# Kernel tuning notes

Measured on AMD Instinct MI355X. Metric: run time of the kernel, lower is better.

Reference implementation:

```python
import jax, jax.numpy as jnp
import numpy as np
from jax import lax

# --- block geometry (matches init_kwargs) ---
B = 8
DIM = 192
HEADS = 6
KEY_DIM = DIM // HEADS  # 32, attn_ratio=1 so d == key_dim and dh == DIM
HX, WX = 32, 32         # search region
HZ, WZ = 16, 16         # template region
T = 1                   # template_number
L = HX * WX + T * HZ * WZ  # 1280 tokens
MLP_HIDDEN = int(DIM * 4.0)
BN_EPS = 1e-5


def _build_bias_idx():
    """Replicates Attention.__init__ global_att=True bias-index construction.
    Unique-offset ids may be permuted vs torch dict-insertion order, which is an
    equivalent reparameterization of the (randomly initialized) bias table."""
    g = np.stack(np.meshgrid(np.arange(HX), np.arange(WX), indexing='ij'), -1).reshape(-1, 2)
    pts = [g]
    for i in range(T):
        r = np.arange(HX + HZ * i, WX + WZ * (i + 1))
        g2 = np.stack(np.meshgrid(r, r, indexing='ij'), -1).reshape(-1, 2)
        pts.append(g2)
    p = np.concatenate(pts, 0)                      # (L, 2)
    off = np.abs(p[:, None, :] - p[None, :, :])     # (L, L, 2)
    key = off[:, :, 0].astype(np.int64) * 4096 + off[:, :, 1]
    uniq, inv = np.unique(key, return_inverse=True)
    return inv.reshape(L, L).astype(np.int32), int(len(uniq))


def setup_inputs() -> dict:
    key = jax.random.key(0)
    ks = jax.random.split(key, 16)
    idx_np, n_off = _build_bias_idx()
    s = 0.02
    return {
        'xz': jax.random.normal(ks[0], (B, L, DIM), jnp.float32),
        'bias_idx': jnp.asarray(idx_np),
        'ln1_g': jnp.ones((DIM,), jnp.float32),
        'ln1_b': jnp.zeros((DIM,), jnp.float32),
        'wqkv': jax.random.normal(ks[1], (DIM, 3 * DIM), jnp.float32) * s,
        'bqkv': jnp.zeros((3 * DIM,), jnp.float32),
        'wproj': jax.random.normal(ks[2], (DIM, DIM), jnp.float32) * s,
        'bproj': jnp.zeros((DIM,), jnp.float32),
        'bias_table': jax.random.normal(ks[3], (HEADS, n_off), jnp.float32) * 0.1,
        'conv_w': jax.random.normal(ks[4], (3, 3, 1, DIM), jnp.float32) * 0.1,  # depthwise HWIO
        'bn_scale': jnp.ones((DIM,), jnp.float32) + jax.random.normal(ks[5], (DIM,), jnp.float32) * 0.01,
        'bn_bias': jax.random.normal(ks[6], (DIM,), jnp.float32) * 0.01,
        'ln2_g': jnp.ones((DIM,), jnp.float32),
        'ln2_b': jnp.zeros((DIM,), jnp.float32),
        'w1': jax.random.normal(ks[7], (DIM, MLP_HIDDEN), jnp.float32) * s,
        'b1': jnp.zeros((MLP_HIDDEN,), jnp.float32),
        'w2': jax.random.normal(ks[8], (MLP_HIDDEN, DIM), jnp.float32) * s,
        'b2': jnp.zeros((DIM,), jnp.float32),
    }


def _layernorm(x, g, b, eps=1e-5):
    mu = jnp.mean(x, -1, keepdims=True)
    var = jnp.mean(jnp.square(x - mu), -1, keepdims=True)
    return (x - mu) * lax.rsqrt(var + eps) * g + b


def reference(xz, bias_idx, ln1_g, ln1_b, wqkv, bqkv, wproj, bproj, bias_table,
              conv_w, bn_scale, bn_bias, ln2_g, ln2_b, w1, b1, w2, b2):
    Bn, N, D = xz.shape
    scale = KEY_DIM ** -0.5
    # --- Attention (LeViT-style with gathered relative-position bias) ---
    h = _layernorm(xz, ln1_g, ln1_b)
    qkv = (h @ wqkv + bqkv).reshape(Bn, N, HEADS, 3 * KEY_DIM)
    q, k, v = jnp.split(qkv, 3, axis=3)            # each (B, N, H, key_dim)
    bias = bias_table[:, bias_idx]                  # (H, N, N) gather
    attn = jnp.einsum('bnhd,bmhd->bhnm', q, k) * scale + bias
    attn = jax.nn.softmax(attn, axis=-1)
    o = jnp.einsum('bhnm,bmhd->bnhd', attn, v).reshape(Bn, N, D)
    xm = xz + o @ wproj + bproj
    # --- depthwise local conv (Conv2d_BN, BN folded to scale/bias) per segment ---
    segs = []
    start = 0
    for (Hh, Ww) in [(HX, WX)] + [(HZ, WZ)] * T:
        xc = xm[:, start:start + Hh * Ww, :].reshape(Bn, Hh, Ww, D)
        xc = lax.conv_general_dilated(
            xc, conv_w, window_strides=(1, 1), padding='SAME',
            dimension_numbers=('NHWC', 'HWIO', 'NHWC'), feature_group_count=D)
        xc = xc * bn_scale + bn_bias
        segs.append(xc.reshape(Bn, Hh * Ww, D))
        start += Hh * Ww
    xm = jnp.concatenate(segs, axis=1)
    # --- MLP with pre-LN (exact GELU, matching nn.GELU default) ---
    m = _layernorm(xm, ln2_g, ln2_b)
    m = jax.nn.gelu(m @ w1 + b1, approximate=False) @ w2 + b2
    return xm + m
```

## Files before the change

kernel.cpp:

```cpp
#include <hip/hip_runtime.h>
#include <hip/hip_bf16.h>

#define BATCH 8
#define LTOK 1280
#define DIMC 192
#define HEADS 6
#define KD 32
#define HID 768
#define NROWS (BATCH*LTOK)

typedef short s16x8 __attribute__((ext_vector_type(8)));
typedef float f32x4 __attribute__((ext_vector_type(4)));
typedef unsigned short u16;

#define QS (0.17677669529663687f * 1.4426950408889634f)
#define L2E 1.4426950408889634f

__device__ __forceinline__ u16 f2bf(float x) {
    unsigned u = __float_as_uint(x);
    u = (u + 0x7FFFu + ((u >> 16) & 1u)) >> 16;
    return (u16)u;
}
__device__ __forceinline__ float bflo(unsigned u) { return __uint_as_float(u << 16); }
__device__ __forceinline__ float bfhi(unsigned u) { return __uint_as_float(u & 0xffff0000u); }
__device__ __forceinline__ float fexp2(float x) { float r; asm("v_exp_f32 %0, %1" : "=v"(r) : "v"(x)); return r; }
__device__ __forceinline__ float frcp(float x)  { float r; asm("v_rcp_f32 %0, %1" : "=v"(r) : "v"(x)); return r; }

__global__ __launch_bounds__(256) void pre_a(const float* __restrict__ w0,
                                             u16* __restrict__ o0,
                                             const float* __restrict__ xz,
                                             const float* __restrict__ ln1g,
                                             const float* __restrict__ ln1b,
                                             u16* __restrict__ hbuf) {
    __shared__ float s[16][17];
    int f = blockIdx.x;
    if (f >= 432) {
        int row = (f - 432) * 4 + (threadIdx.x >> 6);
        int lane = threadIdx.x & 63;
        const float* xr = xz + (size_t)row * DIMC;
        float v0 = xr[lane], v1 = xr[lane + 64], v2 = xr[lane + 128];
        float sm = v0 + v1 + v2;
        float ss = v0 * v0 + v1 * v1 + v2 * v2;
        #pragma unroll
        for (int off = 32; off; off >>= 1) {
            sm += __shfl_xor(sm, off);
            ss += __shfl_xor(ss, off);
        }
        float mu  = sm * (1.0f / DIMC);
        float var = ss * (1.0f / DIMC) - mu * mu;
        float inv = rsqrtf(var + 1e-5f);
        u16* yr = hbuf + (size_t)row * DIMC;
        yr[lane]       = f2bf((v0 - mu) * inv * ln1g[lane]       + ln1b[lane]);
        yr[lane + 64]  = f2bf((v1 - mu) * inv * ln1g[lane + 64]  + ln1b[lane + 64]);
        yr[lane + 128] = f2bf((v2 - mu) * inv * ln1g[lane + 128] + ln1b[lane + 128]);
        return;
    }
    int tn = f % 36, tk = f / 36;
    int tx = threadIdx.x & 15, ty = threadIdx.x >> 4;
    s[ty][tx] = w0[(size_t)(tk * 16 + ty) * 576 + tn * 16 + tx];
    __syncthreads();
    o0[(size_t)(tn * 16 + ty) * 192 + tk * 16 + tx] = f2bf(s[tx][ty]);
}

__global__ __launch_bounds__(256) void qkv_mega(const u16* __restrict__ A,
                                                const u16* __restrict__ Wt,
                                                const float* __restrict__ bias,
                                                u16* __restrict__ qb,
                                                u16* __restrict__ kp,
                                                u16* __restrict__ vp,
                                                const int* __restrict__ bidx,
                                                const float* __restrict__ btab,
                                                int n_off, u16* __restrict__ bmp,
                                                const float* __restrict__ wp,
                                                const float* __restrict__ wf1,
                                                const float* __restrict__ wf2,
                                                u16* __restrict__ op,
                                                u16* __restrict__ of1,
                                                u16* __restrict__ of2) {
    int bid = blockIdx.x;
    if (bid >= 9960) {
        __shared__ float s[16][17];
        int f2 = bid - 9960;
        const float* in; u16* out; int K, N, tn, tk;
        if (f2 < 144)      { in = wp;  out = op;  K = 192; N = 192; tn = f2 % 12; tk = f2 / 12; }
        else if (f2 < 720) { in = wf1; out = of1; K = 192; N = 768; int q = f2 - 144; tn = q % 48; tk = q / 48; }
        else               { in = wf2; out = of2; K = 768; N = 192; int q = f2 - 720; tn = q % 12; tk = q / 12; }
        int tx = threadIdx.x & 15, ty = threadIdx.x >> 4;
        s[ty][tx] = in[(size_t)(tk * 16 + ty) * N + tn * 16 + tx];
        __syncthreads();
        out[(size_t)(tn * 16 + ty) * K + tk * 16 + tx] = f2bf(s[tx][ty]);
        return;
    }
    if (bid >= 360) {
        int fb = bid - 360;
        int qt = fb / 120;
        int rem = fb - qt * 120;
        int T = rem / 6, h = rem - (rem / 6) * 6;
        int tid = threadIdx.x;
        int half = tid >> 7, L = (tid >> 1) & 63, j4 = (tid & 1) * 4;
        int n = qt * 16 + (L & 15);
        int m = T * 64 + half * 32 + ((L >> 4) << 3) + j4;
        int4 iv = *(const int4*)(bidx + (size_t)n * LTOK + m);
        const float* tab = btab + (size_t)h * n_off;
        ushort4 o;
        o.x = f2bf(tab[iv.x] * L2E);
        o.y = f2bf(tab[iv.y] * L2E);
        o.z = f2bf(tab[iv.z] * L2E);
        o.w = f2bf(tab[iv.w] * L2E);
        *(ushort4*)(bmp + (size_t)(h * 80 + qt) * 20480 + T * 1024 + tid * 4) = o;
        return;
    }
    int bx = bid % 9, by = bid / 9;
    int tid = threadIdx.x;
    int L = tid & 63, w = tid >> 6;
    int r = L & 15, g = L >> 4;
    int m0 = by * 256 + w * 64;
    int n0 = bx * 64;

    f32x4 acc[4][4] = {};
    const u16* Ab = A + (size_t)(m0 + r) * 192 + g * 8;
    const u16* Wb = Wt + (size_t)(n0 + r) * 192 + g * 8;
    #pragma unroll 6
    for (int k0 = 0; k0 < 192; k0 += 32) {
        s16x8 af[4];
        #pragma unroll
        for (int mi = 0; mi < 4; ++mi)
            af[mi] = *(const s16x8*)(Ab + (size_t)mi * 16 * 192 + k0);
        #pragma unroll
        for (int nn = 0; nn < 4; ++nn) {
            s16x8 bf = *(const s16x8*)(Wb + (size_t)nn * 16 * 192 + k0);
            #pragma unroll
            for (int mi = 0; mi < 4; ++mi)
                acc[mi][nn] = __builtin_amdgcn_mfma_f32_16x16x32_bf16(af[mi], bf, acc[mi][nn], 0, 0, 0);
        }
    }
    #pragma unroll
    for (int mi = 0; mi < 4; ++mi)
    #pragma unroll
    for (int nn = 0; nn < 4; ++nn) {
        int cb = n0 + nn * 16;
        int h  = cb / 96, c0 = cb % 96;
        int reg = c0 >> 5;
        #pragma unroll
        for (int i = 0; i < 4; ++i) {
            int row = m0 + mi * 16 + g * 4 + i;
            float v = acc[mi][nn][i] + bias[cb + r];
            if (reg == 0) {
                v *= QS;
                qb[(size_t)row * DIMC + h * 32 + (c0 & 31) + r] = f2bf(v);
            } else {
                int b_ = row / LTOK, t = row - b_ * LTOK;
                int T = t >> 5, it = t & 31;
                int d = (c0 & 31) + r;
                if (reg == 1) {
                    int which = (it >> 2) & 1;
                    int ik = ((it >> 3) << 2) | (it & 3);
                    int Lk = ((d >> 3) << 4) + ik;
                    kp[((size_t)(b_ * HEADS + h) * 40 + T) * 1024 + which * 512 + Lk * 8 + (d & 7)] = f2bf(v);
                } else {
                    int Lv = ((it >> 3) << 4) + (d & 15);
                    vp[((size_t)(b_ * HEADS + h) * 40 + T) * 1024 + (d >> 4) * 512 + Lv * 8 + (it & 7)] = f2bf(v);
                }
            }
        }
    }
}

template<int ACT, int RES, int OBF, int K, int MTILE>
__global__ __launch_bounds__(256) void gemm_mfma(const u16* __restrict__ A,
                                                 const u16* __restrict__ Wt,
                                                 const float* __restrict__ bias,
                                                 const float* __restrict__ R,
                                                 void* __restrict__ Cp,
                                                 int N) {
    constexpr int SUB = MTILE / 64;
    int tid = threadIdx.x;
    int L = tid & 63, w = tid >> 6;
    int r = L & 15, g = L >> 4;
    int m0 = blockIdx.y * MTILE + w * (16 * SUB);
    int n0 = blockIdx.x * 64;

    f32x4 acc[SUB][4] = {};
    const u16* Ab = A + (size_t)(m0 + r) * K + g * 8;
    const u16* Wb = Wt + (size_t)(n0 + r) * K + g * 8;
    #pragma unroll 6
    for (int k0 = 0; k0 < K; k0 += 32) {
        s16x8 af[SUB];
        #pragma unroll
        for (int mi = 0; mi < SUB; ++mi)
            af[mi] = *(const s16x8*)(Ab + (size_t)mi * 16 * K + k0);
        #pragma unroll
        for (int nn = 0; nn < 4; ++nn) {
            s16x8 bf = *(const s16x8*)(Wb + (size_t)nn * 16 * K + k0);
            #pragma unroll
            for (int mi = 0; mi < SUB; ++mi)
                acc[mi][nn] = __builtin_amdgcn_mfma_f32_16x16x32_bf16(af[mi], bf, acc[mi][nn], 0, 0, 0);
        }
    }

    #pragma unroll
    for (int mi = 0; mi < SUB; ++mi)
    #pragma unroll
    for (int nn = 0; nn < 4; ++nn) {
        int cb = n0 + nn * 16;
        #pragma unroll
        for (int i = 0; i < 4; ++i) {
            int row = m0 + mi * 16 + g * 4 + i;
            float v = acc[mi][nn][i] + bias[cb + r];
            if (ACT == 1) {
                float u = v;
                float y = 0.7978845608028654f * (u + 0.044715f * u * u * u);
                float e2 = fexp2(y * 2.885390081777927f);
                v = u - u * frcp(e2 + 1.0f);
            }
            if (RES) v += R[(size_t)row * N + cb + r];
            if (OBF) ((u16*)Cp)[(size_t)row * N + cb + r] = f2bf(v);
            else     ((float*)Cp)[(size_t)row * N + cb + r] = v;
        }
    }
}

__global__ __launch_bounds__(256) void attn_mfma(const u16* __restrict__ qb,
                                                 const u16* __restrict__ kp,
                                                 const u16* __restrict__ vp,
                                                 const u16* __restrict__ bmp,
                                                 u16* __restrict__ ob) {
    __shared__ __align__(16) u16 kvs[2][2][2048];
    int tid = threadIdx.x;
    int L = tid & 63, w = tid >> 6;
    int r = L & 15, g = L >> 4;
    int L8 = L * 8;

    int bid = blockIdx.x;
    int work = (bid & 7) * 120 + (bid >> 3);
    int b  = work & 7;
    int hq = work >> 3;
    int qt = (hq % 20) * 4 + w;
    int h  = hq / 20;

    s16x8 qf = *(const s16x8*)(qb + (size_t)(b * LTOK + qt * 16 + r) * DIMC + h * 32 + g * 8);

    int skv = w >> 1, half = w & 1;
    const u16* gs = (skv ? vp : kp) + (size_t)(b * HEADS + h) * 40 * 1024 + L8;
    u16* dst0 = &kvs[0][skv][half * 1024 + L8];
    u16* dst1 = &kvs[1][skv][half * 1024 + L8];

    const u16* bmr = bmp + (size_t)(h * 80 + qt) * 20480 + L8;

    f32x4 acc0 = {0.f, 0.f, 0.f, 0.f}, acc1 = {0.f, 0.f, 0.f, 0.f};
    float lsum = 0.f;

    {
        int4 pA = *(const int4*)(gs + half * 1024);
        int4 pB = *(const int4*)(gs + half * 1024 + 512);
        *(int4*)dst0 = pA;
        *(int4*)(dst0 + 512) = pB;
    }
    int4 cb0 = *(const int4*)(bmr);
    int4 cb1 = *(const int4*)(bmr + 512);
    __syncthreads();

    f32x4 s0, s1, s2, s3;
    {
        const u16* kb = &kvs[0][0][0];
        f32x4 z0, z1, z2, z3;
        z0[0] = bflo(cb0.x); z0[1] = bfhi(cb0.x); z0[2] = bflo(cb0.y); z0[3] = bfhi(cb0.y);
        z1[0] = bflo(cb0.z); z1[1] = bfhi(cb0.z); z1[2] = bflo(cb0.w); z1[3] = bfhi(cb0.w);
        z2[0] = bflo(cb1.x); z2[1] = bfhi(cb1.x); z2[2] = bflo(cb1.y); z2[3] = bfhi(cb1.y);
        z3[0] = bflo(cb1.z); z3[1] = bfhi(cb1.z); z3[2] = bflo(cb1.w); z3[3] = bfhi(cb1.w);
        s16x8 kf0 = *(const s16x8*)(kb + L8);
        s16x8 kf1 = *(const s16x8*)(kb + 512 + L8);
        s16x8 kf2 = *(const s16x8*)(kb + 1024 + L8);
        s16x8 kf3 = *(const s16x8*)(kb + 1536 + L8);
        s0 = __builtin_amdgcn_mfma_f32_16x16x32_bf16(kf0, qf, z0, 0, 0, 0);
        s1 = __builtin_amdgcn_mfma_f32_16x16x32_bf16(kf1, qf, z1, 0, 0, 0);
        s2 = __builtin_amdgcn_mfma_f32_16x16x32_bf16(kf2, qf, z2, 0, 0, 0);
        s3 = __builtin_amdgcn_mfma_f32_16x16x32_bf16(kf3, qf, z3, 0, 0, 0);
    }

    #pragma unroll 1
    for (int T = 0; T < 20; ++T) {
        int4 nA, nB, nb0, nb1;
        if (T < 19) {
            nA  = *(const int4*)(gs + (size_t)(2 * T + 2 + half) * 1024);
            nB  = *(const int4*)(gs + (size_t)(2 * T + 2 + half) * 1024 + 512);
            nb0 = *(const int4*)(bmr + (size_t)(T + 1) * 1024);
            nb1 = *(const int4*)(bmr + (size_t)(T + 1) * 1024 + 512);
        }
        __builtin_amdgcn_s_setprio(1);
        float p[16];
        #pragma unroll
        for (int j = 0; j < 4; ++j) {
            p[j]      = fexp2(s0[j]);
            p[4 + j]  = fexp2(s1[j]);
            p[8 + j]  = fexp2(s2[j]);
            p[12 + j] = fexp2(s3[j]);
        }
        float t0 = ((p[0] + p[1]) + (p[2] + p[3])) + ((p[4] + p[5]) + (p[6] + p[7]));
        float t1 = ((p[8] + p[9]) + (p[10] + p[11])) + ((p[12] + p[13]) + (p[14] + p[15]));
        lsum += t0 + t1;
        union { unsigned u[4]; s16x8 v; } pa, pb;
        #pragma unroll
        for (int j = 0; j < 4; ++j) {
            asm("v_cvt_pk_bf16_f32 %0, %1, %2" : "=v"(pa.u[j]) : "v"(p[2 * j]), "v"(p[2 * j + 1]));
            asm("v_cvt_pk_bf16_f32 %0, %1, %2" : "=v"(pb.u[j]) : "v"(p[8 + 2 * j]), "v"(p[9 + 2 * j]));
        }
        const u16* vb = &kvs[T & 1][1][0];
        s16x8 v0 = *(const s16x8*)(vb + L8);
        s16x8 v1 = *(const s16x8*)(vb + 512 + L8);
        s16x8 v2 = *(const s16x8*)(vb + 1024 + L8);
        s16x8 v3 = *(const s16x8*)(vb + 1536 + L8);
        acc0 = __builtin_amdgcn_mfma_f32_16x16x32_bf16(pa.v, v0, acc0, 0, 0, 0);
        acc1 = __builtin_amdgcn_mfma_f32_16x16x32_bf16(pa.v, v1, acc1, 0, 0, 0);
        acc0 = __builtin_amdgcn_mfma_f32_16x16x32_bf16(pb.v, v2, acc0, 0, 0, 0);
        acc1 = __builtin_amdgcn_mfma_f32_16x16x32_bf16(pb.v, v3, acc1, 0, 0, 0);
        __builtin_amdgcn_s_setprio(0);

        if (T < 19) {
            u16* d = (T & 1) ? dst0 : dst1;
            *(int4*)d = nA;
            *(int4*)(d + 512) = nB;
        }
        __syncthreads();
        if (T < 19) {
            const u16* kb = &kvs[(T + 1) & 1][0][0];
            f32x4 z0, z1, z2, z3;
            z0[0] = bflo(nb0.x); z0[1] = bfhi(nb0.x); z0[2] = bflo(nb0.y); z0[3] = bfhi(nb0.y);
            z1[0] = bflo(nb0.z); z1[1] = bfhi(nb0.z); z1[2] = bflo(nb0.w); z1[3] = bfhi(nb0.w);
            z2[0] = bflo(nb1.x); z2[1] = bfhi(nb1.x); z2[2] = bflo(nb1.y); z2[3] = bfhi(nb1.y);
            z3[0] = bflo(nb1.z); z3[1] = bfhi(nb1.z); z3[2] = bflo(nb1.w); z3[3] = bfhi(nb1.w);
            s16x8 kf0 = *(const s16x8*)(kb + L8);
            s16x8 kf1 = *(const s16x8*)(kb + 512 + L8);
            s16x8 kf2 = *(const s16x8*)(kb + 1024 + L8);
            s16x8 kf3 = *(const s16x8*)(kb + 1536 + L8);
            __builtin_amdgcn_s_setprio(1);
            s0 = __builtin_amdgcn_mfma_f32_16x16x32_bf16(kf0, qf, z0, 0, 0, 0);
            s1 = __builtin_amdgcn_mfma_f32_16x16x32_bf16(kf1, qf, z1, 0, 0, 0);
            s2 = __builtin_amdgcn_mfma_f32_16x16x32_bf16(kf2, qf, z2, 0, 0, 0);
            s3 = __builtin_amdgcn_mfma_f32_16x16x32_bf16(kf3, qf, z3, 0, 0, 0);
            __builtin_amdgcn_s_setprio(0);
        }
    }

    float lr = lsum;
    lr += __shfl_xor(lr, 16);
    lr += __shfl_xor(lr, 32);
    #pragma unroll
    for (int i = 0; i < 4; ++i) {
        float linv = frcp(__shfl(lr, 4 * g + i));
        size_t orow = (size_t)(b * LTOK + qt * 16 + 4 * g + i) * DIMC + h * 32 + r;
        ob[orow]      = f2bf(acc0[i] * linv);
        ob[orow + 16] = f2bf(acc1[i] * linv);
    }
}

__global__ __launch_bounds__(256) void conv_ln_kernel(const float* __restrict__ xm,
                                                      const float* __restrict__ w,
                                                      const float* __restrict__ scale,
                                                      const float* __restrict__ bias,
                                                      const float* __restrict__ g2,
                                                      const float* __restrict__ b2,
                                                      float* __restrict__ xm2,
                                                      u16* __restrict__ y) {
    int row = blockIdx.x * 4 + (threadIdx.x >> 6);
    int lane = threadIdx.x & 63;
    int b = row / LTOK, t = row - b * LTOK;
    int H, W, base, y0, x0;
    if (t < 1024) { H = 32; W = 32; base = 0;    y0 = t >> 5;            x0 = t & 31; }
    else          { H = 16; W = 16; base = 1024; int tt = t - 1024; y0 = tt >> 4; x0 = tt & 15; }
    float a0 = 0.f, a1 = 0.f, a2 = 0.f;
    #pragma unroll
    for (int ky = 0; ky < 3; ++ky) {
        int yy = y0 + ky - 1;
        if (yy < 0 || yy >= H) continue;
        #pragma unroll
        for (int kx = 0; kx < 3; ++kx) {
            int xx = x0 + kx - 1;
            if (xx < 0 || xx >= W) continue;
            const float* xr = xm + (size_t)(b * LTOK + base + yy * W + xx) * DIMC;
            const float* wr = w + (ky * 3 + kx) * DIMC;
            a0 += wr[lane]       * xr[lane];
            a1 += wr[lane + 64]  * xr[lane + 64];
            a2 += wr[lane + 128] * xr[lane + 128];
        }
    }
    float v0 = a0 * scale[lane]       + bias[lane];
    float v1 = a1 * scale[lane + 64]  + bias[lane + 64];
    float v2 = a2 * scale[lane + 128] + bias[lane + 128];
    float* xr2 = xm2 + (size_t)row * DIMC;
    xr2[lane] = v0; xr2[lane + 64] = v1; xr2[lane + 128] = v2;
    float s = v0 + v1 + v2;
    float ss = v0 * v0 + v1 * v1 + v2 * v2;
    #pragma unroll
    for (int off = 32; off; off >>= 1) {
        s  += __shfl_xor(s, off);
        ss += __shfl_xor(ss, off);
    }
    float mu  = s * (1.0f / DIMC);
    float var = ss * (1.0f / DIMC) - mu * mu;
    float inv = rsqrtf(var + 1e-5f);
    u16* yr = y + (size_t)row * DIMC;
    yr[lane]       = f2bf((v0 - mu) * inv * g2[lane]       + b2[lane]);
    yr[lane + 64]  = f2bf((v1 - mu) * inv * g2[lane + 64]  + b2[lane + 64]);
    yr[lane + 128] = f2bf((v2 - mu) * inv * g2[lane + 128] + b2[lane + 128]);
}

extern "C" void kernel_launch(void* const* d_in, const int* in_sizes, int n_in,
                              void* d_out, int out_size, void* d_ws, size_t ws_size,
                              hipStream_t stream) {
    const float* xz       = (const float*)d_in[0];
    const int*   bidx     = (const int*)  d_in[1];
    const float* ln1_g    = (const float*)d_in[2];
    const float* ln1_b    = (const float*)d_in[3];
    const float* wqkv     = (const float*)d_in[4];
    const float* bqkv     = (const float*)d_in[5];
    const float* wproj    = (const float*)d_in[6];
    const float* bproj    = (const float*)d_in[7];
    const float* btab     = (const float*)d_in[8];
    const float* conv_w   = (const float*)d_in[9];
    const float* bn_scale = (const float*)d_in[10];
    const float* bn_bias  = (const float*)d_in[11];
    const float* ln2_g    = (const float*)d_in[12];
    const float* ln2_b    = (const float*)d_in[13];
    const float* w1       = (const float*)d_in[14];
    const float* b1       = (const float*)d_in[15];
    const float* w2       = (const float*)d_in[16];
    const float* b2       = (const float*)d_in[17];
    int n_off = in_sizes[8] / HEADS;
    float* out = (float*)d_out;

    char* wsb = (char*)d_ws;
    u16*  hbuf   = (u16*)(wsb + 0);
    u16*  ob     = (u16*)(wsb + 0);
    u16*  wqkvT  = (u16*)(wsb + 3932160);
    u16*  wprojT = (u16*)(wsb + 4153344);
    u16*  w1T    = (u16*)(wsb + 4227072);
    u16*  w2T    = (u16*)(wsb + 4521984);
    u16*  bmp    = (u16*)(wsb + 4816896);
    u16*  hid    = (u16*)(wsb + 4816896);
    u16*  kp     = (u16*)(wsb + 24477696);
    u16*  vp     = (u16*)(wsb + 28409856);
    float* xm2   = (float*)(wsb + 24477696);
    u16*  qb     = (u16*)(wsb + 32342016);
    float* xm    = (float*)(wsb + 32342016);

    pre_a<<<432 + NROWS / 4, 256, 0, stream>>>(wqkv, wqkvT, xz, ln1_g, ln1_b, hbuf);
    qkv_mega<<<11256, 256, 0, stream>>>(
        hbuf, wqkvT, bqkv, qb, kp, vp,
        bidx, btab, n_off, bmp,
        wproj, w1, w2, wprojT, w1T, w2T);
    attn_mfma<<<960, 256, 0, stream>>>(qb, kp, vp, bmp, ob);
    gemm_mfma<0,1,0,DIMC,128><<<dim3(DIMC / 64, NROWS / 128), 256, 0, stream>>>(
        ob, wprojT, bproj, xz, xm, DIMC);
    conv_ln_kernel<<<NROWS / 4, 256, 0, stream>>>(
        xm, conv_w, bn_scale, bn_bias, ln2_g, ln2_b, xm2, hbuf);
    gemm_mfma<1,0,1,DIMC,256><<<dim3(HID / 64, NROWS / 256), 256, 0, stream>>>(
        hbuf, w1T, b1, nullptr, hid, HID);
    gemm_mfma<0,1,0,HID,128><<<dim3(DIMC / 64, NROWS / 128), 256, 0, stream>>>(
        hid, w2T, b2, xm2, out, DIMC);
}
```

Measured before the change: 120.5 us.

## Fuse post-attention tail into one cooperative kernel with grid syncs

Replaces the four tail launches (projection GEMM, conv+LN, MLP fc1 with GELU, fc2) with a single cooperative kernel of 480 blocks that separates the stages with grid-wide barriers. The goal is to remove kernel launch gaps and the tail effects between the dependent stages. The tiles are re-partitioned: the projection uses 64-row tiles, the conv loops over rows, fc1 does two tiles per block and fc2 runs on only 240 blocks. LN2 output moves to a new workspace buffer. The cost is grid.sync overhead and a smaller, fixed grid that may lower occupancy, and the code falls back to separate launches if the cooperative launch fails.

```diff
diff --git a/kernel.cpp b/kernel.cpp
--- a/kernel.cpp
+++ b/kernel.cpp
@@ -1,5 +1,8 @@
 #include <hip/hip_runtime.h>
 #include <hip/hip_bf16.h>
+#include <hip/hip_cooperative_groups.h>
+
+namespace cg = cooperative_groups;
 
 #define BATCH 8
 #define LTOK 1280
@@ -166,60 +169,6 @@
     }
 }
 
-template<int ACT, int RES, int OBF, int K, int MTILE>
-__global__ __launch_bounds__(256) void gemm_mfma(const u16* __restrict__ A,
-                                                 const u16* __restrict__ Wt,
-                                                 const float* __restrict__ bias,
-                                                 const float* __restrict__ R,
-                                                 void* __restrict__ Cp,
-                                                 int N) {
-    constexpr int SUB = MTILE / 64;
-    int tid = threadIdx.x;
-    int L = tid & 63, w = tid >> 6;
-    int r = L & 15, g = L >> 4;
-    int m0 = blockIdx.y * MTILE + w * (16 * SUB);
-    int n0 = blockIdx.x * 64;
-
-    f32x4 acc[SUB][4] = {};
-    const u16* Ab = A + (size_t)(m0 + r) * K + g * 8;
-    const u16* Wb = Wt + (size_t)(n0 + r) * K + g * 8;
-    #pragma unroll 6
-    for (int k0 = 0; k0 < K; k0 += 32) {
-        s16x8 af[SUB];
-        #pragma unroll
-        for (int mi = 0; mi < SUB; ++mi)
-            af[mi] = *(const s16x8*)(Ab + (size_t)mi * 16 * K + k0);
-        #pragma unroll
-        for (int nn = 0; nn < 4; ++nn) {
-            s16x8 bf = *(const s16x8*)(Wb + (size_t)nn * 16 * K + k0);
-            #pragma unroll
-            for (int mi = 0; mi < SUB; ++mi)
-                acc[mi][nn] = __builtin_amdgcn_mfma_f32_16x16x32_bf16(af[mi], bf, acc[mi][nn], 0, 0, 0);
-        }
-    }
-
-    #pragma unroll
-    for (int mi = 0; mi < SUB; ++mi)
-    #pragma unroll
-    for (int nn = 0; nn < 4; ++nn) {
-        int cb = n0 + nn * 16;
-        #pragma unroll
-        for (int i = 0; i < 4; ++i) {
-            int row = m0 + mi * 16 + g * 4 + i;
-            float v = acc[mi][nn][i] + bias[cb + r];
-            if (ACT == 1) {
-                float u = v;
-                float y = 0.7978845608028654f * (u + 0.044715f * u * u * u);
-                float e2 = fexp2(y * 2.885390081777927f);
-                v = u - u * frcp(e2 + 1.0f);
-            }
-            if (RES) v += R[(size_t)row * N + cb + r];
-            if (OBF) ((u16*)Cp)[(size_t)row * N + cb + r] = f2bf(v);
-            else     ((float*)Cp)[(size_t)row * N + cb + r] = v;
-        }
-    }
-}
-
 __global__ __launch_bounds__(256) void attn_mfma(const u16* __restrict__ qb,
                                                  const u16* __restrict__ kp,
                                                  const u16* __restrict__ vp,
@@ -354,6 +303,112 @@
     }
 }
 
+template<int ACT, int RES, int OBF, int K, int SUB>
+__device__ __forceinline__ void gemm_tile(const u16* A, const u16* Wt,
+                                          const float* bias, const float* R,
+                                          void* Cp, int N, int m0b, int n0) {
+    int tid = threadIdx.x;
+    int L = tid & 63, w = tid >> 6;
+    int r = L & 15, g = L >> 4;
+    int m0 = m0b + w * (16 * SUB);
+
+    f32x4 acc[SUB][4] = {};
+    const u16* Ab = A + (size_t)(m0 + r) * K + g * 8;
+    const u16* Wb = Wt + (size_t)(n0 + r) * K + g * 8;
+    #pragma unroll 6
+    for (int k0 = 0; k0 < K; k0 += 32) {
+        s16x8 af[SUB];
+        #pragma unroll
+        for (int mi = 0; mi < SUB; ++mi)
+            af[mi] = *(const s16x8*)(Ab + (size_t)mi * 16 * K + k0);
+        #pragma unroll
+        for (int nn = 0; nn < 4; ++nn) {
+            s16x8 bf = *(const s16x8*)(Wb + (size_t)nn * 16 * K + k0);
+            #pragma unroll
+            for (int mi = 0; mi < SUB; ++mi)
+                acc[mi][nn] = __builtin_amdgcn_mfma_f32_16x16x32_bf16(af[mi], bf, acc[mi][nn], 0, 0, 0);
+        }
+    }
+    #pragma unroll
+    for (int mi = 0; mi < SUB; ++mi)
+    #pragma unroll
+    for (int nn = 0; nn < 4; ++nn) {
+        int cb = n0 + nn * 16;
+        #pragma unroll
+        for (int i = 0; i < 4; ++i) {
+            int row = m0 + mi * 16 + g * 4 + i;
+            float v = acc[mi][nn][i] + bias[cb + r];
+            if (ACT == 1) {
+                float u = v;
+                float y = 0.7978845608028654f * (u + 0.044715f * u * u * u);
+                float e2 = fexp2(y * 2.885390081777927f);
+                v = u - u * frcp(e2 + 1.0f);
+            }
+            if (RES) v += R[(size_t)row * N + cb + r];
+            if (OBF) ((u16*)Cp)[(size_t)row * N + cb + r] = f2bf(v);
+            else     ((float*)Cp)[(size_t)row * N + cb + r] = v;
+        }
+    }
+}
+
+template<int ACT, int RES, int OBF, int K, int MTILE>
+__global__ __launch_bounds__(256) void gemm_mfma(const u16* __restrict__ A,
+                                                 const u16* __restrict__ Wt,
+                                                 const float* __restrict__ bias,
+                                                 const float* __restrict__ R,
+                                                 void* __restrict__ Cp,
+                                                 int N) {
+    gemm_tile<ACT, RES, OBF, K, MTILE / 64>(A, Wt, bias, R, Cp, N,
+                                            blockIdx.y * MTILE, blockIdx.x * 64);
+}
+
+__device__ __forceinline__ void conv_ln_body(const float* xm, const float* w,
+                                             const float* scale, const float* bias,
+                                             const float* g2, const float* b2,
+                                             float* xm2, u16* y, int grp) {
+    int row = grp * 4 + (threadIdx.x >> 6);
+    int lane = threadIdx.x & 63;
+    int b = row / LTOK, t = row - b * LTOK;
+    int H, W, base, y0, x0;
+    if (t < 1024) { H = 32; W = 32; base = 0;    y0 = t >> 5;            x0 = t & 31; }
+    else          { H = 16; W = 16; base = 1024; int tt = t - 1024; y0 = tt >> 4; x0 = tt & 15; }
+    float a0 = 0.f, a1 = 0.f, a2 = 0.f;
+    #pragma unroll
+    for (int ky = 0; ky < 3; ++ky) {
+        int yy = y0 + ky - 1;
+        if (yy < 0 || yy >= H) continue;
+        #pragma unroll
+        for (int kx = 0; kx < 3; ++kx) {
+            int xx = x0 + kx - 1;
+            if (xx < 0 || xx >= W) continue;
+            const float* xr = xm + (size_t)(b * LTOK + base + yy * W + xx) * DIMC;
+            const float* wr = w + (ky * 3 + kx) * DIMC;
+            a0 += wr[lane]       * xr[lane];
+            a1 += wr[lane + 64]  * xr[lane + 64];
+            a2 += wr[lane + 128] * xr[lane + 128];
+        }
+    }
+    float v0 = a0 * scale[lane]       + bias[lane];
+    float v1 = a1 * scale[lane + 64]  + bias[lane + 64];
+    float v2 = a2 * scale[lane + 128] + bias[lane + 128];
+    float* xr2 = xm2 + (size_t)row * DIMC;
+    xr2[lane] = v0; xr2[lane + 64] = v1; xr2[lane + 128] = v2;
+    float s = v0 + v1 + v2;
+    float ss = v0 * v0 + v1 * v1 + v2 * v2;
+    #pragma unroll
+    for (int off = 32; off; off >>= 1) {
+        s  += __shfl_xor(s, off);
+        ss += __shfl_xor(ss, off);
+    }
+    float mu  = s * (1.0f / DIMC);
+    float var = ss * (1.0f / DIMC) - mu * mu;
+    float inv = rsqrtf(var + 1e-5f);
+    u16* yr = y + (size_t)row * DIMC;
+    yr[lane]       = f2bf((v0 - mu) * inv * g2[lane]       + b2[lane]);
+    yr[lane + 64]  = f2bf((v1 - mu) * inv * g2[lane + 64]  + b2[lane + 64]);
+    yr[lane + 128] = f2bf((v2 - mu) * inv * g2[lane + 128] + b2[lane + 128]);
+}
+
 __global__ __launch_bounds__(256) void conv_ln_kernel(const float* __restrict__ xm,
                                                       const float* __restrict__ w,
                                                       const float* __restrict__ scale,
@@ -362,47 +417,52 @@
                                                       const float* __restrict__ b2,
                                                       float* __restrict__ xm2,
                                                       u16* __restrict__ y) {
-    int row = blockIdx.x * 4 + (threadIdx.x >> 6);
-    int lane = threadIdx.x & 63;
-    int b = row / LTOK, t = row - b * LTOK;
-    int H, W, base, y0, x0;
-    if (t < 1024) { H = 32; W = 32; base = 0;    y0 = t >> 5;            x0 = t & 31; }
-    else          { H = 16; W = 16; base = 1024; int tt = t - 1024; y0 = tt >> 4; x0 = tt & 15; }
-    float a0 = 0.f, a1 = 0.f, a2 = 0.f;
-    #pragma unroll
-    for (int ky = 0; ky < 3; ++ky) {
-        int yy = y0 + ky - 1;
-        if (yy < 0 || yy >= H) continue;
-        #pragma unroll
-        for (int kx = 0; kx < 3; ++kx) {
-            int xx = x0 + kx - 1;
-            if (xx < 0 || xx >= W) continue;
-            const float* xr = xm + (size_t)(b * LTOK + base + yy * W + xx) * DIMC;
-            const float* wr = w + (ky * 3 + kx) * DIMC;
-            a0 += wr[lane]       * xr[lane];
-            a1 += wr[lane + 64]  * xr[lane + 64];
-            a2 += wr[lane + 128] * xr[lane + 128];
-        }
-    }
-    float v0 = a0 * scale[lane]       + bias[lane];
-    float v1 = a1 * scale[lane + 64]  + bias[lane + 64];
-    float v2 = a2 * scale[lane + 128] + bias[lane + 128];
-    float* xr2 = xm2 + (size_t)row * DIMC;
-    xr2[lane] = v0; xr2[lane + 64] = v1; xr2[lane + 128] = v2;
-    float s = v0 + v1 + v2;
-    float ss = v0 * v0 + v1 * v1 + v2 * v2;
-    #pragma unroll
-    for (int off = 32; off; off >>= 1) {
-        s  += __shfl_xor(s, off);
-        ss += __shfl_xor(ss, off);
-    }
-    float mu  = s * (1.0f / DIMC);
-    float var = ss * (1.0f / DIMC) - mu * mu;
-    float inv = rsqrtf(var + 1e-5f);
-    u16* yr = y + (size_t)row * DIMC;
-    yr[lane]       = f2bf((v0 - mu) * inv * g2[lane]       + b2[lane]);
-    yr[lane + 64]  = f2bf((v1 - mu) * inv * g2[lane + 64]  + b2[lane + 64]);
-    yr[lane + 128] = f2bf((v2 - mu) * inv * g2[lane + 128] + b2[lane + 128]);
+    conv_ln_body(xm, w, scale, bias, g2, b2, xm2, y, blockIdx.x);
+}
+
+__global__ __launch_bounds__(256) void tail_kernel(const u16* ob,
+                                                   const u16* wprojT,
+                                                   const float* bproj,
+                                                   const float* xz,
+                                                   float* xm,
+                                                   const float* conv_w,
+                                                   const float* bn_scale,
+                                                   const float* bn_bias,
+                                                   const float* ln2g,
+                                                   const float* ln2b,
+                                                   float* xm2,
+                                                   u16* hbuf2,
+                                                   const u16* w1T,
+                                                   const float* b1,
+                                                   u16* hid,
+                                                   const u16* w2T,
+                                                   const float* b2,
+                                                   float* out) {
+    cg::grid_group grid = cg::this_grid();
+    int bid = blockIdx.x;
+
+    {
+        int bx = bid % 3, by = bid / 3;
+        gemm_tile<0, 1, 0, DIMC, 1>(ob, wprojT, bproj, xz, xm, DIMC, by * 64, bx * 64);
+    }
+    grid.sync();
+
+    for (int it = bid; it < NROWS / 4; it += 480)
+        conv_ln_body(xm, conv_w, bn_scale, bn_bias, ln2g, ln2b, xm2, hbuf2, it);
+    grid.sync();
+
+    #pragma unroll
+    for (int i = 0; i < 2; ++i) {
+        int it = bid + i * 480;
+        int bx = it % 12, by = it / 12;
+        gemm_tile<1, 0, 1, DIMC, 2>(hbuf2, w1T, b1, nullptr, hid, HID, by * 128, bx * 64);
+    }
+    grid.sync();
+
+    if (bid < 240) {
+        int bx = bid % 3, by = bid / 3;
+        gemm_tile<0, 1, 0, HID, 2>(hid, w2T, b2, xm2, out, DIMC, by * 128, bx * 64);
+    }
 }
 
 extern "C" void kernel_launch(void* const* d_in, const int* in_sizes, int n_in,
@@ -443,6 +503,7 @@
     float* xm2   = (float*)(wsb + 24477696);
     u16*  qb     = (u16*)(wsb + 32342016);
     float* xm    = (float*)(wsb + 32342016);
+    u16*  hbuf2  = (u16*)(wsb + 40206336);
 
     pre_a<<<432 + NROWS / 4, 256, 0, stream>>>(wqkv, wqkvT, xz, ln1_g, ln1_b, hbuf);
     qkv_mega<<<11256, 256, 0, stream>>>(
@@ -450,12 +511,25 @@
         bidx, btab, n_off, bmp,
         wproj, w1, w2, wprojT, w1T, w2T);
     attn_mfma<<<960, 256, 0, stream>>>(qb, kp, vp, bmp, ob);
-    gemm_mfma<0,1,0,DIMC,128><<<dim3(DIMC / 64, NROWS / 128), 256, 0, stream>>>(
-        ob, wprojT, bproj, xz, xm, DIMC);
-    conv_ln_kernel<<<NROWS / 4, 256, 0, stream>>>(
-        xm, conv_w, bn_scale, bn_bias, ln2_g, ln2_b, xm2, hbuf);
-    gemm_mfma<1,0,1,DIMC,256><<<dim3(HID / 64, NROWS / 256), 256, 0, stream>>>(
-        hbuf, w1T, b1, nullptr, hid, HID);
-    gemm_mfma<0,1,0,HID,128><<<dim3(DIMC / 64, NROWS / 128), 256, 0, stream>>>(
-        hid, w2T, b2, xm2, out, DIMC);
-}
+    {
+        void* ta[18];
+        ta[0]  = (void*)&ob;       ta[1]  = (void*)&wprojT;  ta[2]  = (void*)&bproj;
+        ta[3]  = (void*)&xz;       ta[4]  = (void*)&xm;      ta[5]  = (void*)&conv_w;
+        ta[6]  = (void*)&bn_scale; ta[7]  = (void*)&bn_bias; ta[8]  = (void*)&ln2_g;
+        ta[9]  = (void*)&ln2_b;    ta[10] = (void*)&xm2;     ta[11] = (void*)&hbuf2;
+        ta[12] = (void*)&w1T;      ta[13] = (void*)&b1;      ta[14] = (void*)&hid;
+        ta[15] = (void*)&w2T;      ta[16] = (void*)&b2;      ta[17] = (void*)&out;
+        hipError_t err = hipLaunchCooperativeKernel(
+            reinterpret_cast<void*>(tail_kernel), dim3(480), dim3(256), ta, 0, stream);
+        if (err != hipSuccess) {
+            gemm_mfma<0,1,0,DIMC,128><<<dim3(3, 80), 256, 0, stream>>>(
+                ob, wprojT, bproj, xz, xm, DIMC);
+            conv_ln_kernel<<<NROWS / 4, 256, 0, stream>>>(
+                xm, conv_w, bn_scale, bn_bias, ln2_g, ln2_b, xm2, hbuf2);
+            gemm_mfma<1,0,1,DIMC,256><<<dim3(12, 40), 256, 0, stream>>>(
+                hbuf2, w1T, b1, nullptr, hid, HID);
+            gemm_mfma<0,1,0,HID,128><<<dim3(3, 80), 256, 0, stream>>>(
+                hid, w2T, b2, xm2, out, DIMC);
+        }
+    }
+}
```

After: 327.9 us. 2.72x slower.
